# Kernel tuning notes

Measured on AMD Instinct MI355X. Metric: run time of the kernel, lower is better.

## Reference

```python
import jax, jax.numpy as jnp
import numpy as np

B, N, M, D, F, L = 128, 512, 512, 256, 512, 5
EPS = 1e-5  # torch InstanceNorm1d default eps


def setup_inputs() -> dict:
    key = jax.random.key(0)
    ks = jax.random.split(key, 12)
    s_d = 1.0 / np.sqrt(D)
    s_f = 1.0 / np.sqrt(F)
    return {
        "row_emb": jax.random.normal(ks[0], (B, N, D), jnp.float32),
        "col_emb": jax.random.normal(ks[1], (B, M, D), jnp.float32),
        "cost_mat": jax.random.uniform(ks[2], (B, N, M), jnp.float32),
        "log_scale": jnp.float32(np.log2(N)),
        "Wq": jax.random.normal(ks[3], (L, 2, D, D), jnp.float32) * s_d,
        "Wk": jax.random.normal(ks[4], (L, 2, D, D), jnp.float32) * s_d,
        "Wv": jax.random.normal(ks[5], (L, 2, D, D), jnp.float32) * s_d,
        "g1": jnp.ones((L, 2, D), jnp.float32),
        "be1": jnp.zeros((L, 2, D), jnp.float32),
        "W1": jax.random.normal(ks[6], (L, 2, D, F), jnp.float32) * s_d,
        "b1": jnp.zeros((L, 2, F), jnp.float32),
        "W2": jax.random.normal(ks[7], (L, 2, F, D), jnp.float32) * s_f,
        "b2": jnp.zeros((L, 2, D), jnp.float32),
        "g2": jnp.ones((L, 2, D), jnp.float32),
        "be2": jnp.zeros((L, 2, D), jnp.float32),
        "alpha": jnp.ones((L, 2), jnp.float32),
    }


def _instance_norm(x, g, b):
    # x: (B, seq, D); normalize over seq per (batch, channel), affine over D
    mu = x.mean(axis=1, keepdims=True)
    var = jnp.mean(jnp.square(x - mu), axis=1, keepdims=True)
    return (x - mu) * jax.lax.rsqrt(var + EPS) * g + b


def _aft(q, k, v, adaptation_bias):
    # Attention-free mixing: exp(bias) shared across numerator/denominator GEMMs
    E = jnp.exp(adaptation_bias)          # (B, n, m)
    ek = jnp.exp(k)                       # (B, m, D)
    num = jnp.einsum('bnm,bmd->bnd', E, ek * v)
    den = jnp.einsum('bnm,bmd->bnd', E, ek)
    weighted = jnp.nan_to_num(num / den)  # matches torch nan/inf safety net
    return jax.nn.sigmoid(q) * weighted


def _enc_block(xr, xc, cm, Wq, Wk, Wv, g1, be1, W1, b1, W2, b2, g2, be2, alpha):
    q = xr @ Wq
    k = xc @ Wk
    v = xc @ Wv
    out_aft = _aft(q, k, v, alpha * cm)
    h1 = _instance_norm(xr + out_aft, g1, be1)
    ff = jax.nn.relu(h1 @ W1 + b1) @ W2 + b2
    return _instance_norm(h1 + ff, g2, be2)


def reference(row_emb, col_emb, cost_mat, log_scale, Wq, Wk, Wv,
              g1, be1, W1, b1, W2, b2, g2, be2, alpha):
    cm = (-log_scale) * cost_mat          # (B, N, M)
    cmT = jnp.swapaxes(cm, 1, 2)          # (B, M, N)
    for l in range(L):
        new_row = _enc_block(row_emb, col_emb, cm,
                             Wq[l, 0], Wk[l, 0], Wv[l, 0], g1[l, 0], be1[l, 0],
                             W1[l, 0], b1[l, 0], W2[l, 0], b2[l, 0],
                             g2[l, 0], be2[l, 0], alpha[l, 0])
        new_col = _enc_block(col_emb, row_emb, cmT,
                             Wq[l, 1], Wk[l, 1], Wv[l, 1], g1[l, 1], be1[l, 1],
                             W1[l, 1], b1[l, 1], W2[l, 1], b2[l, 1],
                             g2[l, 1], be2[l, 1], alpha[l, 1])
        row_emb, col_emb = new_row, new_col
    return (row_emb, col_emb)
```

## Files before the change

### kernel.cpp

```cpp
#include <hip/hip_runtime.h>

typedef unsigned short u16;
typedef __attribute__((ext_vector_type(8))) short short8;
typedef __attribute__((ext_vector_type(4))) float f32x4;

#define DEVFUN __device__ __forceinline__

namespace {

constexpr int kB = 128;
constexpr int kN = 512;
constexpr int kD = 256;
constexpr int kF = 512;
constexpr int kL = 5;
constexpr float kEPS = 1e-5f;
constexpr long BND = (long)kB * kN * kD;

DEVFUN float bf2f(u16 u) {
  unsigned v = ((unsigned)u) << 16;
  float f;
  __builtin_memcpy(&f, &v, 4);
  return f;
}
DEVFUN u16 f2bf(float f) {
  unsigned x;
  __builtin_memcpy(&x, &f, 4);
  x = (x + 0x7FFFu + ((x >> 16) & 1u)) >> 16;
  return (u16)x;
}
DEVFUN u16 f2h(float f) {
  _Float16 h = (_Float16)f;
  u16 u;
  __builtin_memcpy(&u, &h, 2);
  return u;
}
DEVFUN float h2f(u16 u) {
  _Float16 h;
  __builtin_memcpy(&h, &u, 2);
  return (float)h;
}
DEVFUN float fsig(float x) { return 1.f / (1.f + __expf(-x)); }

union Pk8 { u16 p[8]; uint4 v; };
union Pk4 { u16 p[4]; uint2 v; };

DEVFUN void gload16(const u16* g, u16* l) {
  __builtin_amdgcn_global_load_lds(
      (const __attribute__((address_space(1))) void*)g,
      (__attribute__((address_space(3))) void*)l, 16, 0, 0);
}

DEVFUN void waitv8() { asm volatile("s_waitcnt vmcnt(8)" ::: "memory"); }
DEVFUN void waitv0() { asm volatile("s_waitcnt vmcnt(0)" ::: "memory"); }

template <int MODE>
__global__ __launch_bounds__(256) void tcvt(const float* __restrict__ src,
                                            u16* __restrict__ dst, int R,
                                            int C, const float* __restrict__ al,
                                            int pi, const float* __restrict__ ls) {
  __shared__ u16 T[64 * 64];
  const int t = threadIdx.x;
  const long z = blockIdx.z;
  const int cBase = blockIdx.x * 64, rBase = blockIdx.y * 64;
  float s = 0.f;
  if constexpr (MODE == 1) s = -al[pi] * ls[0];
#pragma unroll
  for (int i = 0; i < 4; ++i) {
    int u = i * 256 + t;
    int n = u >> 4, m4 = u & 15;
    float4 v = *(const float4*)(src + (z * R + rBase + n) * C + cBase + m4 * 4);
    Pk4 pk;
    if constexpr (MODE == 1) {
      pk.p[0] = f2bf(__expf(s * v.x)); pk.p[1] = f2bf(__expf(s * v.y));
      pk.p[2] = f2bf(__expf(s * v.z)); pk.p[3] = f2bf(__expf(s * v.w));
    } else if constexpr (MODE == 2) {
      pk.p[0] = f2h(v.x); pk.p[1] = f2h(v.y);
      pk.p[2] = f2h(v.z); pk.p[3] = f2h(v.w);
    } else {
      pk.p[0] = f2bf(v.x); pk.p[1] = f2bf(v.y);
      pk.p[2] = f2bf(v.z); pk.p[3] = f2bf(v.w);
    }
    int ch = (m4 >> 1) ^ ((n >> 3) & 7), hf = m4 & 1;
    *(uint2*)&T[n * 64 + ch * 8 + hf * 4] = pk.v;
  }
  __syncthreads();
#pragma unroll
  for (int j = 0; j < 2; ++j) {
    int u = j * 256 + t;
    int om = u >> 3, nc = u & 7;
    Pk8 pk;
#pragma unroll
    for (int i = 0; i < 8; ++i) {
      int n = nc * 8 + i;
      int ch = (om >> 3) ^ ((n >> 3) & 7);
      pk.p[i] = T[n * 64 + ch * 8 + (om & 7)];
    }
    *(uint4*)(dst + (z * C + cBase + om) * R + rBase + nc * 8) = pk.v;
  }
}

__global__ __launch_bounds__(256) void eexp(const float* __restrict__ src,
                                            u16* __restrict__ dst, long n8,
                                            const float* __restrict__ al,
                                            int pi, const float* __restrict__ ls) {
  const float s = -al[pi] * ls[0];
  for (long i = blockIdx.x * 256 + threadIdx.x; i < n8;
       i += (long)gridDim.x * 256) {
    const float* p = src + i * 8;
    float4 v0 = *(const float4*)p, v1 = *(const float4*)(p + 4);
    Pk8 pk;
    pk.p[0] = f2bf(__expf(s * v0.x)); pk.p[1] = f2bf(__expf(s * v0.y));
    pk.p[2] = f2bf(__expf(s * v0.z)); pk.p[3] = f2bf(__expf(s * v0.w));
    pk.p[4] = f2bf(__expf(s * v1.x)); pk.p[5] = f2bf(__expf(s * v1.y));
    pk.p[6] = f2bf(__expf(s * v1.z)); pk.p[7] = f2bf(__expf(s * v1.w));
    *(uint4*)(dst + i * 8) = pk.v;
  }
}

__global__ __launch_bounds__(256) void eexpH(const u16* __restrict__ src,
                                             u16* __restrict__ dst, long n8,
                                             const float* __restrict__ al,
                                             int pi, const float* __restrict__ ls) {
  const float s = -al[pi] * ls[0];
  for (long i = blockIdx.x * 256 + threadIdx.x; i < n8;
       i += (long)gridDim.x * 256) {
    Pk8 h;
    h.v = *(const uint4*)(src + i * 8);
    Pk8 pk;
#pragma unroll
    for (int q = 0; q < 8; ++q) pk.p[q] = f2bf(__expf(s * h2f(h.p[q])));
    *(uint4*)(dst + i * 8) = pk.v;
  }
}

template <int MODE>
__global__ __launch_bounds__(256) void cvtb(const float* __restrict__ src,
                                            u16* __restrict__ dst, long n8) {
  for (long i = blockIdx.x * 256 + threadIdx.x; i < n8;
       i += (long)gridDim.x * 256) {
    const float* p = src + i * 8;
    float4 v0 = *(const float4*)p, v1 = *(const float4*)(p + 4);
    Pk8 pk;
    if constexpr (MODE == 2) {
      pk.p[0] = f2h(v0.x); pk.p[1] = f2h(v0.y);
      pk.p[2] = f2h(v0.z); pk.p[3] = f2h(v0.w);
      pk.p[4] = f2h(v1.x); pk.p[5] = f2h(v1.y);
      pk.p[6] = f2h(v1.z); pk.p[7] = f2h(v1.w);
    } else {
      pk.p[0] = f2bf(v0.x); pk.p[1] = f2bf(v0.y);
      pk.p[2] = f2bf(v0.z); pk.p[3] = f2bf(v0.w);
      pk.p[4] = f2bf(v1.x); pk.p[5] = f2bf(v1.y);
      pk.p[6] = f2bf(v1.z); pk.p[7] = f2bf(v1.w);
    }
    *(uint4*)(dst + i * 8) = pk.v;
  }
}

DEVFUN void mfma_step(const u16* As, const u16* Bs, int wr, int wc, int lr,
                      int lhi, f32x4 acc[4][4]) {
#pragma unroll
  for (int ks = 0; ks < 2; ++ks) {
    short8 af[4], bfr[4];
#pragma unroll
    for (int m = 0; m < 4; ++m) {
      int r = wr + m * 16 + lr;
      af[m] = *(const short8*)&As[r * 64 + (((ks << 2) + lhi) ^ (r & 7)) * 8];
    }
#pragma unroll
    for (int n = 0; n < 4; ++n) {
      int r = wc + n * 16 + lr;
      bfr[n] = *(const short8*)&Bs[r * 64 + (((ks << 2) + lhi) ^ (r & 7)) * 8];
    }
#pragma unroll
    for (int m = 0; m < 4; ++m)
#pragma unroll
      for (int n = 0; n < 4; ++n)
        acc[m][n] = __builtin_amdgcn_mfma_f32_16x16x32_bf16(af[m], bfr[n],
                                                            acc[m][n], 0, 0, 0);
  }
}

enum Epi { EP_SIG = 0, EP_RELUB, EP_BIASRES };

template <int EPI, int KK>
__global__ __launch_bounds__(256) void gemm_mf(
    const u16* __restrict__ Asrc, const u16* __restrict__ WT, int gx,
    void* __restrict__ outp, const void* __restrict__ aux,
    const u16* __restrict__ aux2b) {
  __shared__ u16 SM[4 * 8192];
  const int t = threadIdx.x;
  const int lane = t & 63, wid = t >> 6;
  const int lr = lane & 15, lhi = lane >> 4;
  const int wr = (wid >> 1) * 64, wc = (wid & 1) * 64;
  const int cpx = gridDim.x >> 3;
  const int rb = (blockIdx.x & 7) * cpx + (blockIdx.x >> 3);
  const int bx = rb % gx;
  const long rowBase = (long)(rb / gx) * 128;
  const int colBase = bx * 128;
  const int r0 = wid * 32;
  const int rl = lane >> 3, sl = lane & 7;

  f32x4 acc[4][4];
#pragma unroll
  for (int m = 0; m < 4; ++m)
#pragma unroll
    for (int n = 0; n < 4; ++n) acc[m][n] = {0.f, 0.f, 0.f, 0.f};

  auto stage = [&](int tt, int pb) {
    const int kt = tt << 6;
    u16* As = SM + pb * 16384;
    u16* Bs = SM + pb * 16384 + 8192;
#pragma unroll
    for (int j = 0; j < 4; ++j) {
      int r = r0 + j * 8 + rl;
      int gch = sl ^ (r & 7);
      gload16(Asrc + (rowBase + r) * KK + kt + gch * 8, &As[(r0 + j * 8) * 64]);
      gload16(WT + (long)(colBase + r) * KK + kt + gch * 8,
              &Bs[(r0 + j * 8) * 64]);
    }
  };

  constexpr int NT = KK >> 6;
  stage(0, 0);
  stage(1, 1);
  waitv8();
  __builtin_amdgcn_s_barrier();
#pragma unroll
  for (int tt = 0; tt < NT - 1; ++tt) {
    mfma_step(SM + (tt & 1) * 16384, SM + (tt & 1) * 16384 + 8192, wr, wc, lr,
              lhi, acc);
    __builtin_amdgcn_s_barrier();
    if (tt + 2 < NT) {
      stage(tt + 2, tt & 1);
      waitv8();
    } else {
      waitv0();
    }
    __builtin_amdgcn_s_barrier();
  }
  mfma_step(SM + ((NT - 1) & 1) * 16384, SM + ((NT - 1) & 1) * 16384 + 8192,
            wr, wc, lr, lhi, acc);

#pragma unroll
  for (int m = 0; m < 4; ++m) {
#pragma unroll
    for (int n = 0; n < 4; ++n) {
#pragma unroll
      for (int rr = 0; rr < 4; ++rr) {
        float v = acc[m][n][rr];
        long grow = rowBase + wr + m * 16 + lhi * 4 + rr;
        int gcol = colBase + wc + n * 16 + lr;
        if constexpr (EPI == EP_SIG) {
          ((u16*)outp)[grow * 256 + gcol] = f2bf(fsig(v));
        } else if constexpr (EPI == EP_RELUB) {
          float bb = ((const float*)aux)[gcol];
          ((u16*)outp)[grow * 512 + gcol] = f2bf(fmaxf(v + bb, 0.f));
        } else {
          float bb = ((const float*)aux)[gcol];
          ((u16*)outp)[grow * 256 + gcol] =
              f2bf(v + bb + bf2f(aux2b[grow * 256 + gcol]));
        }
      }
    }
  }
}

union KvSm {
  struct { u16 A[128 * 64]; u16 Bk[128 * 64]; u16 Bv[128 * 64]; } s;
  u16 T[128 * 128];
};

__global__ __launch_bounds__(256) void kv_mf(const u16* __restrict__ Asrc,
                                             const u16* __restrict__ WkT,
                                             const u16* __restrict__ WvT,
                                             u16* __restrict__ Cb) {
  __shared__ KvSm sm;
  const int t = threadIdx.x;
  const int lane = t & 63, wid = t >> 6;
  const int lr = lane & 15, lhi = lane >> 4;
  const int wr = (wid >> 1) * 64, wc = (wid & 1) * 64;
  const int cpx = gridDim.x >> 3;
  const int rb = (blockIdx.x & 7) * cpx + (blockIdx.x >> 3);
  const long rowBase = (long)(rb >> 1) * 128;
  const int colBase = (rb & 1) * 128;
  const long b = rowBase >> 9;
  const int mInB = (int)(rowBase & 511);
  const int r0 = wid * 32;
  const int rl = lane >> 3, sl = lane & 7;

  f32x4 ka[4][4], va[4][4];
#pragma unroll
  for (int m = 0; m < 4; ++m)
#pragma unroll
    for (int n = 0; n < 4; ++n) {
      ka[m][n] = {0.f, 0.f, 0.f, 0.f};
      va[m][n] = {0.f, 0.f, 0.f, 0.f};
    }

  for (int kt = 0; kt < 256; kt += 64) {
#pragma unroll
    for (int j = 0; j < 4; ++j) {
      int r = r0 + j * 8 + rl;
      int gch = sl ^ (r & 7);
      gload16(Asrc + (rowBase + r) * 256 + kt + gch * 8,
              &sm.s.A[(r0 + j * 8) * 64]);
      gload16(WkT + (long)(colBase + r) * 256 + kt + gch * 8,
              &sm.s.Bk[(r0 + j * 8) * 64]);
      gload16(WvT + (long)(colBase + r) * 256 + kt + gch * 8,
              &sm.s.Bv[(r0 + j * 8) * 64]);
    }
    __syncthreads();
    mfma_step(sm.s.A, sm.s.Bk, wr, wc, lr, lhi, ka);
    mfma_step(sm.s.A, sm.s.Bv, wr, wc, lr, lhi, va);
    __syncthreads();
  }

#pragma unroll
  for (int pass = 0; pass < 2; ++pass) {
#pragma unroll
    for (int m = 0; m < 4; ++m) {
#pragma unroll
      for (int n = 0; n < 4; ++n) {
        int m0 = wr + m * 16 + lhi * 4;
        int d = wc + n * 16 + lr;
        Pk4 pk;
#pragma unroll
        for (int rr = 0; rr < 4; ++rr) {
          float ek = __expf(ka[m][n][rr]);
          pk.p[rr] = f2bf(pass ? ek * va[m][n][rr] : ek);
        }
        int slot = (m0 >> 3) ^ (d & 7);
        *(uint2*)&sm.T[d * 128 + slot * 8 + (m0 & 7)] = pk.v;
      }
    }
    __syncthreads();
    const long rbase = b * 512 + (pass ? 0 : 256) + colBase;
#pragma unroll
    for (int j = 0; j < 8; ++j) {
      int idx = j * 256 + t;
      int d = idx >> 4, c = idx & 15;
      uint4 v = *(const uint4*)&sm.T[d * 128 + ((c ^ (d & 7)) * 8)];
      *(uint4*)(Cb + (rbase + d) * 512 + mInB + c * 8) = v;
    }
    __syncthreads();
  }
}

union SmU {
  struct { u16 A[128 * 64]; u16 B[128 * 64]; } s;
  float den[128 * 68];
};

__global__ __launch_bounds__(256) void aft_mf(
    const u16* __restrict__ Ebuf, const u16* __restrict__ CbufT,
    const u16* __restrict__ qb, const u16* __restrict__ xrB,
    u16* __restrict__ dst) {
  __shared__ SmU sm;
  const int t = threadIdx.x;
  const int lane = t & 63, wid = t >> 6;
  const int lr = lane & 15, lhi = lane >> 4;
  const int wr = (wid >> 1) * 64, wc = (wid & 1) * 64;
  const int rb = (blockIdx.x & 7) * 256 + (blockIdx.x >> 3);
  const long b = rb >> 4;
  const int nBase = ((rb >> 2) & 3) * 128;
  const int dBase = (rb & 3) * 64;
  const int r0 = wid * 32;
  const int rl = lane >> 3, sl = lane & 7;

  f32x4 acc[4][4];
#pragma unroll
  for (int m = 0; m < 4; ++m)
#pragma unroll
    for (int n = 0; n < 4; ++n) acc[m][n] = {0.f, 0.f, 0.f, 0.f};

  for (int kt = 0; kt < 512; kt += 64) {
#pragma unroll
    for (int j = 0; j < 4; ++j) {
      int r = r0 + j * 8 + rl;
      int gch = sl ^ (r & 7);
      gload16(Ebuf + (b * 512 + nBase + r) * 512 + kt + gch * 8,
              &sm.s.A[(r0 + j * 8) * 64]);
      int gslot = (r < 64) ? (dBase + r) : (256 + dBase + (r - 64));
      gload16(CbufT + (b * 512 + gslot) * 512 + kt + gch * 8,
              &sm.s.B[(r0 + j * 8) * 64]);
    }
    __syncthreads();
    mfma_step(sm.s.A, sm.s.B, wr, wc, lr, lhi, acc);
    __syncthreads();
  }

  if (wc == 64) {
#pragma unroll
    for (int m = 0; m < 4; ++m)
#pragma unroll
      for (int n = 0; n < 4; ++n)
#pragma unroll
        for (int rr = 0; rr < 4; ++rr) {
          int nl = wr + m * 16 + lhi * 4 + rr;
          int dl = n * 16 + lr;
          sm.den[nl * 68 + dl] = acc[m][n][rr];
        }
  }
  __syncthreads();
  if (wc == 0) {
#pragma unroll
    for (int m = 0; m < 4; ++m)
#pragma unroll
      for (int n = 0; n < 4; ++n)
#pragma unroll
        for (int rr = 0; rr < 4; ++rr) {
          int nl = wr + m * 16 + lhi * 4 + rr;
          int dl = n * 16 + lr;
          float dv = sm.den[nl * 68 + dl];
          float w = acc[m][n][rr] / dv;
          if (!(w == w)) w = 0.f;
          else if (w > 3.402823466e38f) w = 3.402823466e38f;
          else if (w < -3.402823466e38f) w = -3.402823466e38f;
          long grow = b * 512 + nBase + nl;
          int gcol = dBase + dl;
          float sq = bf2f(qb[grow * 256 + gcol]);
          dst[grow * 256 + gcol] =
              f2bf(bf2f(xrB[grow * 256 + gcol]) + sq * w);
        }
  }
}

template <bool LASTF32>
__global__ __launch_bounds__(256) void inormB(const u16* __restrict__ Xin,
                                              const float* __restrict__ g,
                                              const float* __restrict__ be,
                                              u16* __restrict__ Xb,
                                              float* __restrict__ Xf) {
  const int b = blockIdx.x;
  const int ch0 = blockIdx.y * 64;
  const int t = threadIdx.x;
  const int lc = t & 63;
  const int ch = ch0 + lc;
  const int nr = t >> 6;
  const long base = (long)b * kN * kD + ch;

  float sum = 0.f, sq = 0.f;
  for (int n = nr; n < kN; n += 4) {
    float x = bf2f(Xin[base + (long)n * kD]);
    sum += x;
    sq += x * x;
  }
  __shared__ float s1[4][64], s2[4][64];
  __shared__ float mu[64], rs[64], gg[64], bb[64];
  s1[nr][lc] = sum;
  s2[nr][lc] = sq;
  __syncthreads();
  if (t < 64) {
    float ssum = s1[0][t] + s1[1][t] + s1[2][t] + s1[3][t];
    float ssq = s2[0][t] + s2[1][t] + s2[2][t] + s2[3][t];
    float m = ssum * (1.f / kN);
    float v = ssq * (1.f / kN) - m * m;
    mu[t] = m;
    rs[t] = rsqrtf(v + kEPS);
    gg[t] = g[ch0 + t];
    bb[t] = be[ch0 + t];
  }
  __syncthreads();
  const float m = mu[lc], rr = rs[lc], G = gg[lc], Bt = bb[lc];
  for (int n = nr; n < kN; n += 4) {
    long idx = base + (long)n * kD;
    float y = (bf2f(Xin[idx]) - m) * rr * G + Bt;
    Xb[idx] = f2bf(y);
    if constexpr (LASTF32) Xf[idx] = y;
  }
}

}

extern "C" void kernel_launch(void* const* d_in, const int* in_sizes, int n_in,
                              void* d_out, int out_size, void* d_ws,
                              size_t ws_size, hipStream_t stream) {
  (void)in_sizes; (void)n_in; (void)out_size;

  const float* in_row = (const float*)d_in[0];
  const float* in_col = (const float*)d_in[1];
  const float* cost = (const float*)d_in[2];
  const float* lsc = (const float*)d_in[3];
  const float* Wq = (const float*)d_in[4];
  const float* Wk = (const float*)d_in[5];
  const float* Wv = (const float*)d_in[6];
  const float* g1 = (const float*)d_in[7];
  const float* be1 = (const float*)d_in[8];
  const float* W1 = (const float*)d_in[9];
  const float* b1 = (const float*)d_in[10];
  const float* W2 = (const float*)d_in[11];
  const float* b2 = (const float*)d_in[12];
  const float* g2 = (const float*)d_in[13];
  const float* be2 = (const float*)d_in[14];
  const float* alpha = (const float*)d_in[15];

  float* outRow = (float*)d_out;
  float* outCol = outRow + BND;

  u16* qb = (u16*)d_ws;
  u16* h1b = qb;
  u16* CbufT = qb + BND;
  u16* ffmid = CbufT;
  u16* Ebuf = CbufT + 2 * BND;
  u16* bSt = Ebuf + 2 * BND;
  u16* h0b = bSt + 4 * BND;
  u16* h2b = h0b;
  u16* WqT = h0b + BND;
  u16* WkT = WqT + 10L * 256 * 256;
  u16* WvT = WkT + 10L * 256 * 256;
  u16* W1T = WvT + 10L * 256 * 256;
  u16* W2T = W1T + 10L * 512 * 256;
  u16* costTH = W2T + 10L * 256 * 512;
  u16* costH = costTH + 2 * BND;
  const long needElems = (long)(costH - (u16*)d_ws) + 2 * BND;
  const bool haveCH = (long)ws_size >= needElems * 2;

  const dim3 blk(256);
  tcvt<0><<<dim3(4, 4, 10), blk, 0, stream>>>(Wq, WqT, 256, 256, nullptr, 0, nullptr);
  tcvt<0><<<dim3(4, 4, 10), blk, 0, stream>>>(Wk, WkT, 256, 256, nullptr, 0, nullptr);
  tcvt<0><<<dim3(4, 4, 10), blk, 0, stream>>>(Wv, WvT, 256, 256, nullptr, 0, nullptr);
  tcvt<0><<<dim3(8, 4, 10), blk, 0, stream>>>(W1, W1T, 256, 512, nullptr, 0, nullptr);
  tcvt<0><<<dim3(4, 8, 10), blk, 0, stream>>>(W2, W2T, 512, 256, nullptr, 0, nullptr);
  cvtb<0><<<1024, blk, 0, stream>>>(in_row, bSt + 0 * BND, BND / 8);
  cvtb<0><<<1024, blk, 0, stream>>>(in_col, bSt + 1 * BND, BND / 8);
  if (haveCH) {
    tcvt<2><<<dim3(8, 8, 128), blk, 0, stream>>>(cost, costTH, 512, 512,
                                                 nullptr, 0, nullptr);
    cvtb<2><<<2048, blk, 0, stream>>>(cost, costH, 2 * BND / 8);
  }

  for (int l = 0; l < kL; ++l) {
    const int inPar = l & 1, outPar = 1 - inPar;
    const u16* bR = bSt + (inPar * 2 + 0) * BND;
    const u16* bC = bSt + (inPar * 2 + 1) * BND;

    for (int side = 0; side < 2; ++side) {
      const u16* xrB = side ? bC : bR;
      const u16* xcB = side ? bR : bC;
      u16* outB = bSt + (outPar * 2 + side) * BND;
      float* outF = side ? outCol : outRow;
      const int pi = l * 2 + side;

      if (side == 0) {
        if (haveCH)
          eexpH<<<4096, blk, 0, stream>>>(costH, Ebuf, 2 * BND / 8, alpha, pi,
                                          lsc);
        else
          eexp<<<4096, blk, 0, stream>>>(cost, Ebuf, 2 * BND / 8, alpha, pi,
                                         lsc);
      } else if (haveCH) {
        eexpH<<<4096, blk, 0, stream>>>(costTH, Ebuf, 2 * BND / 8, alpha, pi,
                                        lsc);
      } else {
        tcvt<1><<<dim3(8, 8, 128), blk, 0, stream>>>(cost, Ebuf, 512, 512,
                                                     alpha, pi, lsc);
      }

      gemm_mf<EP_SIG, 256><<<1024, blk, 0, stream>>>(
          xrB, WqT + (long)pi * 256 * 256, 2, qb, nullptr, nullptr);
      kv_mf<<<1024, blk, 0, stream>>>(xcB, WkT + (long)pi * 256 * 256,
                                      WvT + (long)pi * 256 * 256, CbufT);
      aft_mf<<<2048, blk, 0, stream>>>(Ebuf, CbufT, qb, xrB, h0b);
      inormB<false><<<dim3(128, 4), blk, 0, stream>>>(h0b, g1 + pi * 256,
                                                      be1 + pi * 256, h1b,
                                                      nullptr);
      gemm_mf<EP_RELUB, 256><<<2048, blk, 0, stream>>>(
          h1b, W1T + (long)pi * 512 * 256, 4, ffmid, b1 + pi * 512, nullptr);
      gemm_mf<EP_BIASRES, 512><<<1024, blk, 0, stream>>>(
          ffmid, W2T + (long)pi * 256 * 512, 2, h2b, b2 + pi * 256, h1b);
      if (l == kL - 1)
        inormB<true><<<dim3(128, 4), blk, 0, stream>>>(h2b, g2 + pi * 256,
                                                       be2 + pi * 256, outB,
                                                       outF);
      else
        inormB<false><<<dim3(128, 4), blk, 0, stream>>>(h2b, g2 + pi * 256,
                                                        be2 + pi * 256, outB,
                                                        nullptr);
    }
  }
}
```

Before: 3.806 ms.

## Fuse exp-bias, Q GEMM and KV GEMM into one heterogeneous launch

```diff
diff --git a/kernel.cpp b/kernel.cpp
--- a/kernel.cpp
+++ b/kernel.cpp
@@ -96,40 +96,6 @@
       pk.p[i] = T[n * 64 + ch * 8 + (om & 7)];
     }
     *(uint4*)(dst + (z * C + cBase + om) * R + rBase + nc * 8) = pk.v;
-  }
-}
-
-__global__ __launch_bounds__(256) void eexp(const float* __restrict__ src,
-                                            u16* __restrict__ dst, long n8,
-                                            const float* __restrict__ al,
-                                            int pi, const float* __restrict__ ls) {
-  const float s = -al[pi] * ls[0];
-  for (long i = blockIdx.x * 256 + threadIdx.x; i < n8;
-       i += (long)gridDim.x * 256) {
-    const float* p = src + i * 8;
-    float4 v0 = *(const float4*)p, v1 = *(const float4*)(p + 4);
-    Pk8 pk;
-    pk.p[0] = f2bf(__expf(s * v0.x)); pk.p[1] = f2bf(__expf(s * v0.y));
-    pk.p[2] = f2bf(__expf(s * v0.z)); pk.p[3] = f2bf(__expf(s * v0.w));
-    pk.p[4] = f2bf(__expf(s * v1.x)); pk.p[5] = f2bf(__expf(s * v1.y));
-    pk.p[6] = f2bf(__expf(s * v1.z)); pk.p[7] = f2bf(__expf(s * v1.w));
-    *(uint4*)(dst + i * 8) = pk.v;
-  }
-}
-
-__global__ __launch_bounds__(256) void eexpH(const u16* __restrict__ src,
-                                             u16* __restrict__ dst, long n8,
-                                             const float* __restrict__ al,
-                                             int pi, const float* __restrict__ ls) {
-  const float s = -al[pi] * ls[0];
-  for (long i = blockIdx.x * 256 + threadIdx.x; i < n8;
-       i += (long)gridDim.x * 256) {
-    Pk8 h;
-    h.v = *(const uint4*)(src + i * 8);
-    Pk8 pk;
-#pragma unroll
-    for (int q = 0; q < 8; ++q) pk.p[q] = f2bf(__expf(s * h2f(h.p[q])));
-    *(uint4*)(dst + i * 8) = pk.v;
   }
 }
 
@@ -183,17 +149,14 @@
 enum Epi { EP_SIG = 0, EP_RELUB, EP_BIASRES };
 
 template <int EPI, int KK>
-__global__ __launch_bounds__(256) void gemm_mf(
-    const u16* __restrict__ Asrc, const u16* __restrict__ WT, int gx,
-    void* __restrict__ outp, const void* __restrict__ aux,
-    const u16* __restrict__ aux2b) {
-  __shared__ u16 SM[4 * 8192];
+DEVFUN void gemm_body(int rb, int gx, u16* SM, const u16* __restrict__ Asrc,
+                      const u16* __restrict__ WT, void* __restrict__ outp,
+                      const void* __restrict__ aux,
+                      const u16* __restrict__ aux2b) {
   const int t = threadIdx.x;
   const int lane = t & 63, wid = t >> 6;
   const int lr = lane & 15, lhi = lane >> 4;
   const int wr = (wid >> 1) * 64, wc = (wid & 1) * 64;
-  const int cpx = gridDim.x >> 3;
-  const int rb = (blockIdx.x & 7) * cpx + (blockIdx.x >> 3);
   const int bx = rb % gx;
   const long rowBase = (long)(rb / gx) * 128;
   const int colBase = bx * 128;
@@ -265,22 +228,30 @@
   }
 }
 
+template <int EPI, int KK>
+__global__ __launch_bounds__(256) void gemm_mf(
+    const u16* __restrict__ Asrc, const u16* __restrict__ WT, int gx,
+    void* __restrict__ outp, const void* __restrict__ aux,
+    const u16* __restrict__ aux2b) {
+  __shared__ u16 SM[4 * 8192];
+  const int cpx = gridDim.x >> 3;
+  const int rb = (blockIdx.x & 7) * cpx + (blockIdx.x >> 3);
+  gemm_body<EPI, KK>(rb, gx, SM, Asrc, WT, outp, aux, aux2b);
+}
+
 union KvSm {
   struct { u16 A[128 * 64]; u16 Bk[128 * 64]; u16 Bv[128 * 64]; } s;
   u16 T[128 * 128];
 };
 
-__global__ __launch_bounds__(256) void kv_mf(const u16* __restrict__ Asrc,
-                                             const u16* __restrict__ WkT,
-                                             const u16* __restrict__ WvT,
-                                             u16* __restrict__ Cb) {
-  __shared__ KvSm sm;
+DEVFUN void kv_body(int rb, KvSm* smp, const u16* __restrict__ Asrc,
+                    const u16* __restrict__ WkT, const u16* __restrict__ WvT,
+                    u16* __restrict__ Cb) {
+  KvSm& sm = *smp;
   const int t = threadIdx.x;
   const int lane = t & 63, wid = t >> 6;
   const int lr = lane & 15, lhi = lane >> 4;
   const int wr = (wid >> 1) * 64, wc = (wid & 1) * 64;
-  const int cpx = gridDim.x >> 3;
-  const int rb = (blockIdx.x & 7) * cpx + (blockIdx.x >> 3);
   const long rowBase = (long)(rb >> 1) * 128;
   const int colBase = (rb & 1) * 128;
   const long b = rowBase >> 9;
@@ -343,6 +314,46 @@
       *(uint4*)(Cb + (rbase + d) * 512 + mInB + c * 8) = v;
     }
     __syncthreads();
+  }
+}
+
+__global__ __launch_bounds__(256) void fused3(
+    const u16* __restrict__ eSrcH, const float* __restrict__ eSrcF,
+    u16* __restrict__ Ebuf, const float* __restrict__ al, int pi,
+    const float* __restrict__ ls, const u16* __restrict__ xrB,
+    const u16* __restrict__ WqT, u16* __restrict__ qb,
+    const u16* __restrict__ xcB, const u16* __restrict__ WkT,
+    const u16* __restrict__ WvT, u16* __restrict__ Cb) {
+  __shared__ u16 SM[4 * 8192];
+  const int type = blockIdx.x % 3;
+  const int bid = blockIdx.x / 3;
+  const int rb = (bid & 7) * 128 + (bid >> 3);
+  if (type == 0) {
+    gemm_body<EP_SIG, 256>(rb, 2, SM, xrB, WqT, qb, nullptr, nullptr);
+  } else if (type == 1) {
+    kv_body(rb, (KvSm*)SM, xcB, WkT, WvT, Cb);
+  } else {
+    if (eSrcH == nullptr && eSrcF == nullptr) return;
+    const float s = -al[pi] * ls[0];
+    const long n8 = 2 * BND / 8;
+    const long stride = 1024L * 256;
+    for (long i = (long)bid * 256 + threadIdx.x; i < n8; i += stride) {
+      Pk8 pk;
+      if (eSrcH != nullptr) {
+        Pk8 h;
+        h.v = *(const uint4*)(eSrcH + i * 8);
+#pragma unroll
+        for (int q = 0; q < 8; ++q) pk.p[q] = f2bf(__expf(s * h2f(h.p[q])));
+      } else {
+        const float* p = eSrcF + i * 8;
+        float4 v0 = *(const float4*)p, v1 = *(const float4*)(p + 4);
+        pk.p[0] = f2bf(__expf(s * v0.x)); pk.p[1] = f2bf(__expf(s * v0.y));
+        pk.p[2] = f2bf(__expf(s * v0.z)); pk.p[3] = f2bf(__expf(s * v0.w));
+        pk.p[4] = f2bf(__expf(s * v1.x)); pk.p[5] = f2bf(__expf(s * v1.y));
+        pk.p[6] = f2bf(__expf(s * v1.z)); pk.p[7] = f2bf(__expf(s * v1.w));
+      }
+      *(uint4*)(Ebuf + i * 8) = pk.v;
+    }
   }
 }
 
@@ -541,25 +552,20 @@
       float* outF = side ? outCol : outRow;
       const int pi = l * 2 + side;
 
-      if (side == 0) {
-        if (haveCH)
-          eexpH<<<4096, blk, 0, stream>>>(costH, Ebuf, 2 * BND / 8, alpha, pi,
-                                          lsc);
-        else
-          eexp<<<4096, blk, 0, stream>>>(cost, Ebuf, 2 * BND / 8, alpha, pi,
-                                         lsc);
-      } else if (haveCH) {
-        eexpH<<<4096, blk, 0, stream>>>(costTH, Ebuf, 2 * BND / 8, alpha, pi,
-                                        lsc);
+      const u16* eH = nullptr;
+      const float* eF = nullptr;
+      if (haveCH) {
+        eH = side ? costTH : costH;
+      } else if (side == 0) {
+        eF = cost;
       } else {
         tcvt<1><<<dim3(8, 8, 128), blk, 0, stream>>>(cost, Ebuf, 512, 512,
                                                      alpha, pi, lsc);
       }
 
-      gemm_mf<EP_SIG, 256><<<1024, blk, 0, stream>>>(
-          xrB, WqT + (long)pi * 256 * 256, 2, qb, nullptr, nullptr);
-      kv_mf<<<1024, blk, 0, stream>>>(xcB, WkT + (long)pi * 256 * 256,
-                                      WvT + (long)pi * 256 * 256, CbufT);
+      fused3<<<3072, blk, 0, stream>>>(
+          eH, eF, Ebuf, alpha, pi, lsc, xrB, WqT + (long)pi * 256 * 256, qb,
+          xcB, WkT + (long)pi * 256 * 256, WvT + (long)pi * 256 * 256, CbufT);
       aft_mf<<<2048, blk, 0, stream>>>(Ebuf, CbufT, qb, xrB, h0b);
       inormB<false><<<dim3(128, 4), blk, 0, stream>>>(h0b, g1 + pi * 256,
                                                       be1 + pi * 256, h1b,
```

After: 4.099 ms. 7.7% more time.

## Fuse instance-norm statistics into producer GEMM epilogues

Applied to the files above, without the earlier changes.

```diff
diff --git a/kernel.cpp b/kernel.cpp
--- a/kernel.cpp
+++ b/kernel.cpp
@@ -186,7 +186,7 @@
 __global__ __launch_bounds__(256) void gemm_mf(
     const u16* __restrict__ Asrc, const u16* __restrict__ WT, int gx,
     void* __restrict__ outp, const void* __restrict__ aux,
-    const u16* __restrict__ aux2b) {
+    const u16* __restrict__ aux2b, float* __restrict__ statsF) {
   __shared__ u16 SM[4 * 8192];
   const int t = threadIdx.x;
   const int lane = t & 63, wid = t >> 6;
@@ -241,6 +241,7 @@
   mfma_step(SM + ((NT - 1) & 1) * 16384, SM + ((NT - 1) & 1) * 16384 + 8192,
             wr, wc, lr, lhi, acc);
 
+  float psum[4] = {0.f, 0.f, 0.f, 0.f}, psq[4] = {0.f, 0.f, 0.f, 0.f};
 #pragma unroll
   for (int m = 0; m < 4; ++m) {
 #pragma unroll
@@ -257,10 +258,38 @@
           ((u16*)outp)[grow * 512 + gcol] = f2bf(fmaxf(v + bb, 0.f));
         } else {
           float bb = ((const float*)aux)[gcol];
-          ((u16*)outp)[grow * 256 + gcol] =
-              f2bf(v + bb + bf2f(aux2b[grow * 256 + gcol]));
+          float y = v + bb + bf2f(aux2b[grow * 256 + gcol]);
+          ((u16*)outp)[grow * 256 + gcol] = f2bf(y);
+          psum[n] += y;
+          psq[n] += y * y;
         }
       }
+    }
+  }
+
+  if constexpr (EPI == EP_BIASRES) {
+    __syncthreads();
+    float* stS = (float*)SM;
+    float* stQ = stS + 8 * 128;
+    const int ctr = (wid >> 1) * 4 + lhi;
+#pragma unroll
+    for (int n = 0; n < 4; ++n) {
+      stS[ctr * 128 + wc + n * 16 + lr] = psum[n];
+      stQ[ctr * 128 + wc + n * 16 + lr] = psq[n];
+    }
+    __syncthreads();
+    if (t < 128) {
+      float s = 0.f, q = 0.f;
+#pragma unroll
+      for (int i = 0; i < 8; ++i) {
+        s += stS[i * 128 + t];
+        q += stQ[i * 128 + t];
+      }
+      const long b = rowBase >> 9;
+      const int rblk = (int)((rowBase >> 7) & 3);
+      const long o = ((b * 4 + rblk) * 256 + colBase + t) * 2;
+      statsF[o] = s;
+      statsF[o + 1] = q;
     }
   }
 }
@@ -348,13 +377,13 @@
 
 union SmU {
   struct { u16 A[128 * 64]; u16 B[128 * 64]; } s;
-  float den[128 * 68];
+  struct { float den[128 * 68]; float st[2][8][64]; } d;
 };
 
 __global__ __launch_bounds__(256) void aft_mf(
     const u16* __restrict__ Ebuf, const u16* __restrict__ CbufT,
     const u16* __restrict__ qb, const u16* __restrict__ xrB,
-    u16* __restrict__ dst) {
+    u16* __restrict__ dst, float* __restrict__ statsF) {
   __shared__ SmU sm;
   const int t = threadIdx.x;
   const int lane = t & 63, wid = t >> 6;
@@ -398,10 +427,11 @@
         for (int rr = 0; rr < 4; ++rr) {
           int nl = wr + m * 16 + lhi * 4 + rr;
           int dl = n * 16 + lr;
-          sm.den[nl * 68 + dl] = acc[m][n][rr];
+          sm.d.den[nl * 68 + dl] = acc[m][n][rr];
         }
   }
   __syncthreads();
+  float psum[4] = {0.f, 0.f, 0.f, 0.f}, psq[4] = {0.f, 0.f, 0.f, 0.f};
   if (wc == 0) {
 #pragma unroll
     for (int m = 0; m < 4; ++m)
@@ -411,7 +441,7 @@
         for (int rr = 0; rr < 4; ++rr) {
           int nl = wr + m * 16 + lhi * 4 + rr;
           int dl = n * 16 + lr;
-          float dv = sm.den[nl * 68 + dl];
+          float dv = sm.d.den[nl * 68 + dl];
           float w = acc[m][n][rr] / dv;
           if (!(w == w)) w = 0.f;
           else if (w > 3.402823466e38f) w = 3.402823466e38f;
@@ -419,14 +449,38 @@
           long grow = b * 512 + nBase + nl;
           int gcol = dBase + dl;
           float sq = bf2f(qb[grow * 256 + gcol]);
-          dst[grow * 256 + gcol] =
-              f2bf(bf2f(xrB[grow * 256 + gcol]) + sq * w);
+          float y = bf2f(xrB[grow * 256 + gcol]) + sq * w;
+          dst[grow * 256 + gcol] = f2bf(y);
+          psum[n] += y;
+          psq[n] += y * y;
         }
   }
+  __syncthreads();
+  if (wc == 0) {
+    const int ctr = (wid >> 1) * 4 + lhi;
+#pragma unroll
+    for (int n = 0; n < 4; ++n) {
+      sm.d.st[0][ctr][n * 16 + lr] = psum[n];
+      sm.d.st[1][ctr][n * 16 + lr] = psq[n];
+    }
+  }
+  __syncthreads();
+  if (t < 64) {
+    float s = 0.f, q = 0.f;
+#pragma unroll
+    for (int i = 0; i < 8; ++i) {
+      s += sm.d.st[0][i][t];
+      q += sm.d.st[1][i][t];
+    }
+    const long o = ((b * 4 + (nBase >> 7)) * 256 + dBase + t) * 2;
+    statsF[o] = s;
+    statsF[o + 1] = q;
+  }
 }
 
 template <bool LASTF32>
-__global__ __launch_bounds__(256) void inormB(const u16* __restrict__ Xin,
+__global__ __launch_bounds__(256) void inormS(const u16* __restrict__ Xin,
+                                              const float* __restrict__ stats,
                                               const float* __restrict__ g,
                                               const float* __restrict__ be,
                                               u16* __restrict__ Xb,
@@ -439,16 +493,13 @@
   const int nr = t >> 6;
   const long base = (long)b * kN * kD + ch;
 
-  float sum = 0.f, sq = 0.f;
-  for (int n = nr; n < kN; n += 4) {
-    float x = bf2f(Xin[base + (long)n * kD]);
-    sum += x;
-    sq += x * x;
-  }
   __shared__ float s1[4][64], s2[4][64];
   __shared__ float mu[64], rs[64], gg[64], bb[64];
-  s1[nr][lc] = sum;
-  s2[nr][lc] = sq;
+  {
+    const long o = (((long)b * 4 + nr) * 256 + ch) * 2;
+    s1[nr][lc] = stats[o];
+    s2[nr][lc] = stats[o + 1];
+  }
   __syncthreads();
   if (t < 64) {
     float ssum = s1[0][t] + s1[1][t] + s1[2][t] + s1[3][t];
@@ -510,7 +561,8 @@
   u16* WvT = WkT + 10L * 256 * 256;
   u16* W1T = WvT + 10L * 256 * 256;
   u16* W2T = W1T + 10L * 512 * 256;
-  u16* costTH = W2T + 10L * 256 * 512;
+  float* statsF = (float*)(W2T + 10L * 256 * 512);
+  u16* costTH = (u16*)(statsF + 128L * 4 * 256 * 2);
   u16* costH = costTH + 2 * BND;
   const long needElems = (long)(costH - (u16*)d_ws) + 2 * BND;
   const bool haveCH = (long)ws_size >= needElems * 2;
@@ -557,25 +609,24 @@
       }
 
       gemm_mf<EP_SIG, 256><<<1024, blk, 0, stream>>>(
-          xrB, WqT + (long)pi * 256 * 256, 2, qb, nullptr, nullptr);
+          xrB, WqT + (long)pi * 256 * 256, 2, qb, nullptr, nullptr, nullptr);
       kv_mf<<<1024, blk, 0, stream>>>(xcB, WkT + (long)pi * 256 * 256,
                                       WvT + (long)pi * 256 * 256, CbufT);
-      aft_mf<<<2048, blk, 0, stream>>>(Ebuf, CbufT, qb, xrB, h0b);
-      inormB<false><<<dim3(128, 4), blk, 0, stream>>>(h0b, g1 + pi * 256,
-                                                      be1 + pi * 256, h1b,
-                                                      nullptr);
+      aft_mf<<<2048, blk, 0, stream>>>(Ebuf, CbufT, qb, xrB, h0b, statsF);
+      inormS<false><<<dim3(128, 4), blk, 0, stream>>>(
+          h0b, statsF, g1 + pi * 256, be1 + pi * 256, h1b, nullptr);
       gemm_mf<EP_RELUB, 256><<<2048, blk, 0, stream>>>(
-          h1b, W1T + (long)pi * 512 * 256, 4, ffmid, b1 + pi * 512, nullptr);
+          h1b, W1T + (long)pi * 512 * 256, 4, ffmid, b1 + pi * 512, nullptr,
+          nullptr);
       gemm_mf<EP_BIASRES, 512><<<1024, blk, 0, stream>>>(
-          ffmid, W2T + (long)pi * 256 * 512, 2, h2b, b2 + pi * 256, h1b);
+          ffmid, W2T + (long)pi * 256 * 512, 2, h2b, b2 + pi * 256, h1b,
+          statsF);
       if (l == kL - 1)
-        inormB<true><<<dim3(128, 4), blk, 0, stream>>>(h2b, g2 + pi * 256,
-                                                       be2 + pi * 256, outB,
-                                                       outF);
+        inormS<true><<<dim3(128, 4), blk, 0, stream>>>(
+            h2b, statsF, g2 + pi * 256, be2 + pi * 256, outB, outF);
       else
-        inormB<false><<<dim3(128, 4), blk, 0, stream>>>(h2b, g2 + pi * 256,
-                                                        be2 + pi * 256, outB,
-                                                        nullptr);
-    }
-  }
-}
+        inormS<false><<<dim3(128, 4), blk, 0, stream>>>(
+            h2b, statsF, g2 + pi * 256, be2 + pi * 256, outB, nullptr);
+    }
+  }
+}
```

New measurement: 3.299 ms. -13.3%, faster.
